# Kernel tuning notes

Measured on AMD Instinct MI355X. Metric: run time of the kernel, lower is better.

The kernel has to match this reference:

```python
import jax, jax.numpy as jnp
import numpy as np
import math

B, S, D, H = 2, 2048, 1024, 16
DK = D // H


def setup_inputs() -> dict:
    key = jax.random.key(0)
    ks = jax.random.split(key, 14)
    inp = {
        "query": jax.random.normal(ks[0], (B, S, D), dtype=jnp.float32),
        "key": jax.random.normal(ks[1], (B, S, D), dtype=jnp.float32),
        "value": jax.random.normal(ks[2], (B, S, D), dtype=jnp.float32),
        "group_prob": jax.random.uniform(ks[3], (B, S, S), dtype=jnp.float32),
        "mask": jax.random.randint(ks[4], (B, S), 0, 2, dtype=jnp.int32),
    }
    scale = 0.02
    inp["Wq"] = jax.random.normal(ks[5], (D, D), dtype=jnp.float32) * scale
    inp["bq"] = jnp.zeros((D,), dtype=jnp.float32)
    inp["Wk"] = jax.random.normal(ks[6], (D, D), dtype=jnp.float32) * scale
    inp["bk"] = jnp.zeros((D,), dtype=jnp.float32)
    inp["Wv"] = jax.random.normal(ks[7], (D, D), dtype=jnp.float32) * scale
    inp["bv"] = jnp.zeros((D,), dtype=jnp.float32)
    inp["Wo"] = jax.random.normal(ks[8], (D, D), dtype=jnp.float32) * scale
    inp["bo"] = jnp.zeros((D,), dtype=jnp.float32)
    return inp


def reference(query, key, value, group_prob, mask, Wq, bq, Wk, bk, Wv, bv, Wo, bo):
    b, s, d = query.shape
    # project and split heads: [B,S,D] -> [B,H,S,DK]
    def proj(x, W, bias):
        return (x @ W.T + bias).reshape(b, s, H, DK).transpose(0, 2, 1, 3)

    q = proj(query, Wq, bq)
    k = proj(key, Wk, bk)
    v = proj(value, Wv, bv)

    scores = jnp.einsum("bhqd,bhkd->bhqk", q, k) / math.sqrt(DK)  # [B,H,S,S]

    # combined mask: padding-row mask OR diagonal (always attend to self)
    eye = jnp.eye(s, dtype=jnp.int32)
    combined = mask[:, None, None, :] | eye[None, None, :, :]  # [B,1,S,S]
    scores = jnp.where(combined == 0, jnp.float32(-1e9), scores)

    p_attn = jax.nn.softmax(scores, axis=-1)
    p_attn = p_attn * group_prob[:, None, :, :]  # post-softmax group scaling

    x = jnp.einsum("bhqk,bhkd->bhqd", p_attn, v)  # [B,H,S,DK]
    x = x.transpose(0, 2, 1, 3).reshape(b, s, d)
    return x @ Wo.T + bo
```

## Files before the change

kernel.cpp:

```cpp
#include <hip/hip_runtime.h>
#include <hip/hip_bf16.h>
#include <stdint.h>

typedef __bf16 bf16x8 __attribute__((ext_vector_type(8)));
typedef float f32x4 __attribute__((ext_vector_type(4)));

__device__ __forceinline__ void gld16(const void* g, void* l) {
  __builtin_amdgcn_global_load_lds(
      (__attribute__((address_space(1))) void*)(uintptr_t)(g),
      (__attribute__((address_space(3))) void*)(l), 16, 0, 0);
}

struct CastArgs {
  const float* src[7];
  __bf16* dst[7];
  int n[7];
};

__global__ __launch_bounds__(256) void cast_bf16_kernel(CastArgs a) {
  const int t = blockIdx.y;
  const int i = (blockIdx.x * 256 + threadIdx.x) * 8;
  if (i >= a.n[t]) return;
  const float4* s = (const float4*)(a.src[t] + i);
  float4 v0 = s[0], v1 = s[1];
  bf16x8 o;
  o[0] = (__bf16)v0.x; o[1] = (__bf16)v0.y; o[2] = (__bf16)v0.z; o[3] = (__bf16)v0.w;
  o[4] = (__bf16)v1.x; o[5] = (__bf16)v1.y; o[6] = (__bf16)v1.z; o[7] = (__bf16)v1.w;
  *(bf16x8*)(a.dst[t] + i) = o;
}

__global__ __launch_bounds__(256) void cast_gp_kernel(const float* __restrict__ src,
                                                      __bf16* __restrict__ dst) {
  const int i = (blockIdx.x * 256 + threadIdx.x) * 8;
  const float4* s = (const float4*)(src + i);
  float4 v0 = s[0], v1 = s[1];
  bf16x8 o;
  o[0] = (__bf16)v0.x; o[1] = (__bf16)v0.y; o[2] = (__bf16)v0.z; o[3] = (__bf16)v0.w;
  o[4] = (__bf16)v1.x; o[5] = (__bf16)v1.y; o[6] = (__bf16)v1.z; o[7] = (__bf16)v1.w;
  *(bf16x8*)(dst + i) = o;
}

struct QkvArgs {
  const __bf16* A[3];
  const __bf16* B[3];
  const float* bias[3];
  __bf16* out[3];
};

__global__ __launch_bounds__(256) void qkv_gemm(QkvArgs args) {
  __shared__ __align__(16) __bf16 As[128 * 32];
  __shared__ __align__(16) __bf16 Bs[128 * 32];
  const int tid = threadIdx.x;
  const int z = blockIdx.y;
  const int bx = blockIdx.x;
  const int m0 = (z < 2 ? (bx >> 3) : (bx & 7)) * 128;
  const int n0 = (z < 2 ? (bx & 7) : (bx >> 3)) * 128;
  const __bf16* A = args.A[z];
  const __bf16* B = args.B[z];
  const float* bias = args.bias[z];
  __bf16* out = args.out[z];
  const float scale = (z == 0) ? 0.125f : 1.0f;

  const int lane = tid & 63, wid = tid >> 6;
  const int wm = (wid & 1) * 64, wn = (wid >> 1) * 64;
  const int l16 = lane & 15, quad = lane >> 4;

  const int sc = (tid & 3) ^ ((tid >> 2) & 3);
  const __bf16* ga = A + (size_t)(m0 + (tid >> 2)) * 1024 + sc * 8;
  const __bf16* gb = B + (size_t)(n0 + (tid >> 2)) * 1024 + sc * 8;
  char* lA = (char*)As + tid * 16;
  char* lB = (char*)Bs + tid * 16;
  const int a_off = (wm + l16) * 64 + ((quad ^ (l16 & 3)) * 16);
  const int b_off = (wn + l16) * 64 + ((quad ^ (l16 & 3)) * 16);

  f32x4 acc[4][4] = {};

  for (int k0 = 0; k0 < 1024; k0 += 32) {
    __syncthreads();
    gld16(ga + k0, lA);
    gld16(ga + k0 + 64 * 1024, lA + 4096);
    gld16(gb + k0, lB);
    gld16(gb + k0 + 64 * 1024, lB + 4096);
    __syncthreads();
    bf16x8 af[4], bfr[4];
#pragma unroll
    for (int mi = 0; mi < 4; ++mi)
      af[mi] = *(const bf16x8*)((const char*)As + a_off + mi * 1024);
#pragma unroll
    for (int ni = 0; ni < 4; ++ni)
      bfr[ni] = *(const bf16x8*)((const char*)Bs + b_off + ni * 1024);
#pragma unroll
    for (int mi = 0; mi < 4; ++mi)
#pragma unroll
      for (int ni = 0; ni < 4; ++ni)
        acc[mi][ni] = __builtin_amdgcn_mfma_f32_16x16x32_bf16(af[mi], bfr[ni],
                                                              acc[mi][ni], 0, 0, 0);
  }

  if (z < 2) {
#pragma unroll
    for (int ni = 0; ni < 4; ++ni) {
      const int col = n0 + wn + ni * 16 + l16;
      const int h = col >> 6, dk = col & 63;
      const float bb = bias[col];
#pragma unroll
      for (int mi = 0; mi < 4; ++mi)
#pragma unroll
        for (int r = 0; r < 4; ++r) {
          const int row = m0 + wm + mi * 16 + quad * 4 + r;
          const int b = row >> 11, s = row & 2047;
          out[((size_t)(b * 16 + h) * 2048 + s) * 64 + dk] =
              (__bf16)((acc[mi][ni][r] + bb) * scale);
        }
    }
  } else {
#pragma unroll
    for (int mi = 0; mi < 4; ++mi)
#pragma unroll
      for (int r = 0; r < 4; ++r) {
        const int rowm = m0 + wm + mi * 16 + quad * 4 + r;
        const int h = rowm >> 6, dk = rowm & 63;
        const float bb = bias[rowm];
#pragma unroll
        for (int ni = 0; ni < 4; ++ni) {
          const int coln = n0 + wn + ni * 16 + l16;
          const int b = coln >> 11, s = coln & 2047;
          out[((size_t)(b * 16 + h) * 64 + dk) * 2048 + s] =
              (__bf16)(acc[mi][ni][r] + bb);
        }
      }
  }
}

__global__ __launch_bounds__(256) void gemm_out(const __bf16* __restrict__ A,
                                                const __bf16* __restrict__ B,
                                                const float* __restrict__ bias,
                                                float* __restrict__ out) {
  __shared__ __align__(16) __bf16 As[128 * 32];
  __shared__ __align__(16) __bf16 Bs[128 * 32];
  const int tid = threadIdx.x;
  const int m0 = blockIdx.y * 128;
  const int n0 = blockIdx.x * 128;
  const int lane = tid & 63, wid = tid >> 6;
  const int wm = (wid & 1) * 64, wn = (wid >> 1) * 64;
  const int l16 = lane & 15, quad = lane >> 4;

  const int sc = (tid & 3) ^ ((tid >> 2) & 3);
  const __bf16* ga = A + (size_t)(m0 + (tid >> 2)) * 1024 + sc * 8;
  const __bf16* gb = B + (size_t)(n0 + (tid >> 2)) * 1024 + sc * 8;
  char* lA = (char*)As + tid * 16;
  char* lB = (char*)Bs + tid * 16;
  const int a_off = (wm + l16) * 64 + ((quad ^ (l16 & 3)) * 16);
  const int b_off = (wn + l16) * 64 + ((quad ^ (l16 & 3)) * 16);

  f32x4 acc[4][4] = {};

  for (int k0 = 0; k0 < 1024; k0 += 32) {
    __syncthreads();
    gld16(ga + k0, lA);
    gld16(ga + k0 + 64 * 1024, lA + 4096);
    gld16(gb + k0, lB);
    gld16(gb + k0 + 64 * 1024, lB + 4096);
    __syncthreads();
    bf16x8 af[4], bfr[4];
#pragma unroll
    for (int mi = 0; mi < 4; ++mi)
      af[mi] = *(const bf16x8*)((const char*)As + a_off + mi * 1024);
#pragma unroll
    for (int ni = 0; ni < 4; ++ni)
      bfr[ni] = *(const bf16x8*)((const char*)Bs + b_off + ni * 1024);
#pragma unroll
    for (int mi = 0; mi < 4; ++mi)
#pragma unroll
      for (int ni = 0; ni < 4; ++ni)
        acc[mi][ni] = __builtin_amdgcn_mfma_f32_16x16x32_bf16(af[mi], bfr[ni],
                                                              acc[mi][ni], 0, 0, 0);
  }

#pragma unroll
  for (int ni = 0; ni < 4; ++ni) {
    const int col = n0 + wn + ni * 16 + l16;
    const float bb = bias[col];
#pragma unroll
    for (int mi = 0; mi < 4; ++mi)
#pragma unroll
      for (int r = 0; r < 4; ++r) {
        const int row = m0 + wm + mi * 16 + quad * 4 + r;
        out[(size_t)row * 1024 + col] = acc[mi][ni][r] + bb;
      }
  }
}

__global__ __launch_bounds__(256) void attn_kernel(
    const __bf16* __restrict__ Qh, const __bf16* __restrict__ Kh,
    const __bf16* __restrict__ Vt, const __bf16* __restrict__ gp16,
    const int* __restrict__ maskp, __bf16* __restrict__ xb) {
  __shared__ __align__(16) __bf16 Qs[64 * 64];
  __shared__ __align__(16) __bf16 Ks[64 * 64];
  __shared__ __align__(16) __bf16 Vs[64 * 64];
  __shared__ __align__(16) __bf16 Ps[4][16 * 64];
  __shared__ unsigned long long mbits[32];

  const int tid = threadIdx.x;
  const int qt = blockIdx.x, bh = blockIdx.y;
  const int b = bh >> 4, h = bh & 15;
  const int q0 = qt * 64;
  const int lane = tid & 63, wid = tid >> 6, l16 = lane & 15, quad = lane >> 4;
  const size_t head_off = (size_t)bh * (2048 * 64);

  const int srow = tid >> 3;
  const int sc8 = (tid & 7) ^ (srow & 7);
  const int fxor = (l16 & 7);

  {
    const __bf16* gq = Qh + head_off + (size_t)(q0 + srow) * 64 + sc8 * 8;
    gld16(gq, (char*)Qs + tid * 16);
    gld16(gq + 32 * 64, (char*)Qs + 4096 + tid * 16);
  }
  {
    const int* mr = maskp + b * 2048;
#pragma unroll
    for (int t = 0; t < 8; ++t) {
      const int kt2 = wid * 8 + t;
      const int mv = mr[kt2 * 64 + lane];
      const unsigned long long bal = __ballot(mv != 0);
      if (lane == 0) mbits[kt2] = bal;
    }
  }
  __syncthreads();
  bf16x8 aq[2];
  aq[0] = *(const bf16x8*)((const char*)Qs + (wid * 16 + l16) * 128 +
                           ((quad ^ fxor) * 16));
  aq[1] = *(const bf16x8*)((const char*)Qs + (wid * 16 + l16) * 128 +
                           (((4 + quad) ^ fxor) * 16));

  f32x4 o[4] = {};
  float lp[4] = {0.f, 0.f, 0.f, 0.f};
  int irow[4];
#pragma unroll
  for (int r = 0; r < 4; ++r) irow[r] = q0 + wid * 16 + quad * 4 + r;

  const __bf16* gk0 = Kh + head_off + (size_t)srow * 64 + sc8 * 8;
  const __bf16* gv0 = Vt + head_off + (size_t)srow * 2048 + sc8 * 8;
  const __bf16* gpl = gp16 + (size_t)b * 2048 * 2048 +
                      (size_t)(q0 + wid * 16 + l16) * 2048 + quad * 8;

  for (int kt = 0; kt < 32; ++kt) {
    __syncthreads();
    gld16(gk0 + kt * 4096, (char*)Ks + tid * 16);
    gld16(gk0 + kt * 4096 + 2048, (char*)Ks + 4096 + tid * 16);
    gld16(gv0 + kt * 64, (char*)Vs + tid * 16);
    gld16(gv0 + kt * 64 + 32 * 2048, (char*)Vs + 4096 + tid * 16);

    bf16x8 g8_0 = *(const bf16x8*)(gpl + kt * 64);
    bf16x8 g8_1 = *(const bf16x8*)(gpl + kt * 64 + 32);

    const unsigned long long sh = mbits[kt] >> l16;
    const uint32_t shlo = (uint32_t)sh, shhi = (uint32_t)(sh >> 32);
    const bool mk[4] = {(shlo & 1) != 0, (shlo & 0x10000u) != 0,
                        (shhi & 1) != 0, (shhi & 0x10000u) != 0};
    __syncthreads();

    f32x4 sc[4] = {};
#pragma unroll
    for (int kh = 0; kh < 2; ++kh)
#pragma unroll
      for (int ni = 0; ni < 4; ++ni) {
        bf16x8 bk = *(const bf16x8*)((const char*)Ks + (ni * 16 + l16) * 128 +
                                     (((kh * 4 + quad) ^ fxor) * 16));
        sc[ni] = __builtin_amdgcn_mfma_f32_16x16x32_bf16(aq[kh], bk, sc[ni], 0, 0, 0);
      }

    float pw[4][4];
    if (kt != qt) {
#pragma unroll
      for (int ni = 0; ni < 4; ++ni)
#pragma unroll
        for (int r = 0; r < 4; ++r) {
          const float e = __expf(sc[ni][r]);
          const float p = mk[ni] ? e : 0.f;
          lp[r] += p;
          pw[ni][r] = p;
        }
    } else {
#pragma unroll
      for (int ni = 0; ni < 4; ++ni)
#pragma unroll
        for (int r = 0; r < 4; ++r) {
          const float e = __expf(sc[ni][r]);
          const bool diag = (ni == wid) && (l16 == quad * 4 + r);
          const float p = (mk[ni] || diag) ? e : 0.f;
          lp[r] += p;
          pw[ni][r] = p;
        }
    }

#pragma unroll
    for (int ni = 0; ni < 4; ++ni)
#pragma unroll
      for (int r = 0; r < 4; ++r) {
        const int prow = quad * 4 + r;
        const int pchunk = (ni * 2 + (l16 >> 3)) ^ (prow & 7);
        *(__bf16*)((char*)&Ps[wid][0] + prow * 128 + pchunk * 16 + (l16 & 7) * 2) =
            (__bf16)pw[ni][r];
      }
    asm volatile("s_waitcnt lgkmcnt(0)" ::: "memory");

#pragma unroll
    for (int kh = 0; kh < 2; ++kh) {
      bf16x8 ap = *(const bf16x8*)((const char*)&Ps[wid][0] + l16 * 128 +
                                   (((kh * 4 + quad) ^ fxor) * 16));
      const bf16x8 g8 = kh ? g8_1 : g8_0;
      bf16x8 apg;
#pragma unroll
      for (int j = 0; j < 8; ++j)
        apg[j] = (__bf16)((float)ap[j] * (float)g8[j]);
#pragma unroll
      for (int ni = 0; ni < 4; ++ni) {
        bf16x8 bv = *(const bf16x8*)((const char*)Vs + (ni * 16 + l16) * 128 +
                                     (((kh * 4 + quad) ^ fxor) * 16));
        o[ni] = __builtin_amdgcn_mfma_f32_16x16x32_bf16(apg, bv, o[ni], 0, 0, 0);
      }
    }
  }

#pragma unroll
  for (int r = 0; r < 4; ++r) {
    lp[r] += __shfl_xor(lp[r], 1);
    lp[r] += __shfl_xor(lp[r], 2);
    lp[r] += __shfl_xor(lp[r], 4);
    lp[r] += __shfl_xor(lp[r], 8);
    lp[r] = 1.f / lp[r];
  }
#pragma unroll
  for (int ni = 0; ni < 4; ++ni) {
    const int dk = ni * 16 + l16;
#pragma unroll
    for (int r = 0; r < 4; ++r) {
      const float val = o[ni][r] * lp[r];
      xb[((size_t)(b * 2048 + irow[r])) * 1024 + h * 64 + dk] = (__bf16)val;
    }
  }
}

extern "C" void kernel_launch(void* const* d_in, const int* in_sizes, int n_in,
                              void* d_out, int out_size, void* d_ws, size_t ws_size,
                              hipStream_t stream) {
  const float* query = (const float*)d_in[0];
  const float* key_  = (const float*)d_in[1];
  const float* value = (const float*)d_in[2];
  const float* gprob = (const float*)d_in[3];
  const int*   maskp = (const int*)d_in[4];
  const float* Wq = (const float*)d_in[5];
  const float* bq = (const float*)d_in[6];
  const float* Wk = (const float*)d_in[7];
  const float* bk = (const float*)d_in[8];
  const float* Wv = (const float*)d_in[9];
  const float* bv = (const float*)d_in[10];
  const float* Wo = (const float*)d_in[11];
  const float* bo = (const float*)d_in[12];

  char* ws = (char*)d_ws;
  const size_t MB = 1 << 20;
  __bf16* qb  = (__bf16*)(ws + 0 * MB);
  __bf16* kb  = (__bf16*)(ws + 8 * MB);
  __bf16* vb  = (__bf16*)(ws + 16 * MB);
  __bf16* Wqb = (__bf16*)(ws + 24 * MB);
  __bf16* Wkb = (__bf16*)(ws + 26 * MB);
  __bf16* Wvb = (__bf16*)(ws + 28 * MB);
  __bf16* Wob = (__bf16*)(ws + 30 * MB);
  __bf16* Qh  = (__bf16*)(ws + 32 * MB);
  __bf16* Kh  = (__bf16*)(ws + 40 * MB);
  __bf16* Vt  = (__bf16*)(ws + 48 * MB);
  __bf16* xb  = (__bf16*)(ws + 56 * MB);
  __bf16* gp16 = (__bf16*)(ws + 0 * MB);

  CastArgs ca;
  ca.src[0] = query; ca.dst[0] = qb;  ca.n[0] = 4194304;
  ca.src[1] = key_;  ca.dst[1] = kb;  ca.n[1] = 4194304;
  ca.src[2] = value; ca.dst[2] = vb;  ca.n[2] = 4194304;
  ca.src[3] = Wq;    ca.dst[3] = Wqb; ca.n[3] = 1048576;
  ca.src[4] = Wk;    ca.dst[4] = Wkb; ca.n[4] = 1048576;
  ca.src[5] = Wv;    ca.dst[5] = Wvb; ca.n[5] = 1048576;
  ca.src[6] = Wo;    ca.dst[6] = Wob; ca.n[6] = 1048576;
  cast_bf16_kernel<<<dim3(2048, 7), 256, 0, stream>>>(ca);

  QkvArgs qa;
  qa.A[0] = qb;  qa.B[0] = Wqb; qa.bias[0] = bq; qa.out[0] = Qh;
  qa.A[1] = kb;  qa.B[1] = Wkb; qa.bias[1] = bk; qa.out[1] = Kh;
  qa.A[2] = Wvb; qa.B[2] = vb;  qa.bias[2] = bv; qa.out[2] = Vt;
  qkv_gemm<<<dim3(256, 3), 256, 0, stream>>>(qa);

  cast_gp_kernel<<<dim3(4096), 256, 0, stream>>>(gprob, gp16);
  attn_kernel<<<dim3(32, 32), 256, 0, stream>>>(Qh, Kh, Vt, gp16, maskp, xb);
  gemm_out<<<dim3(8, 32), 256, 0, stream>>>(xb, Wob, bo, (float*)d_out);
}
```

Measured before the change: 333.5 us.

## Double-buffer K/V tiles, read fp32 group_prob directly, use exp2 with folded scale

The attention loop now double-buffers K and V tiles in LDS and prefetches the next tile and its group_prob values while computing the current one, leaving one barrier per iteration instead of two. The separate group_prob bf16 cast kernel is removed, so attention reads fp32 group_prob directly. This avoids a full write and re-read of the large matrix but doubles the bytes attention loads for it. The log2(e) factor is folded into the Q projection scale so exp2 replaces expf. The extra LDS buffers and prefetch registers may lower occupancy.

After: 323.8 us. 2.9% less time.

```diff
diff --git a/kernel.cpp b/kernel.cpp
--- a/kernel.cpp
+++ b/kernel.cpp
@@ -4,6 +4,8 @@
 
 typedef __bf16 bf16x8 __attribute__((ext_vector_type(8)));
 typedef float f32x4 __attribute__((ext_vector_type(4)));
+
+#define QSCALE 0.1803368801111244f
 
 __device__ __forceinline__ void gld16(const void* g, void* l) {
   __builtin_amdgcn_global_load_lds(
@@ -27,17 +29,6 @@
   o[0] = (__bf16)v0.x; o[1] = (__bf16)v0.y; o[2] = (__bf16)v0.z; o[3] = (__bf16)v0.w;
   o[4] = (__bf16)v1.x; o[5] = (__bf16)v1.y; o[6] = (__bf16)v1.z; o[7] = (__bf16)v1.w;
   *(bf16x8*)(a.dst[t] + i) = o;
-}
-
-__global__ __launch_bounds__(256) void cast_gp_kernel(const float* __restrict__ src,
-                                                      __bf16* __restrict__ dst) {
-  const int i = (blockIdx.x * 256 + threadIdx.x) * 8;
-  const float4* s = (const float4*)(src + i);
-  float4 v0 = s[0], v1 = s[1];
-  bf16x8 o;
-  o[0] = (__bf16)v0.x; o[1] = (__bf16)v0.y; o[2] = (__bf16)v0.z; o[3] = (__bf16)v0.w;
-  o[4] = (__bf16)v1.x; o[5] = (__bf16)v1.y; o[6] = (__bf16)v1.z; o[7] = (__bf16)v1.w;
-  *(bf16x8*)(dst + i) = o;
 }
 
 struct QkvArgs {
@@ -59,7 +50,7 @@
   const __bf16* B = args.B[z];
   const float* bias = args.bias[z];
   __bf16* out = args.out[z];
-  const float scale = (z == 0) ? 0.125f : 1.0f;
+  const float scale = (z == 0) ? QSCALE : 1.0f;
 
   const int lane = tid & 63, wid = tid >> 6;
   const int wm = (wid & 1) * 64, wn = (wid >> 1) * 64;
@@ -193,11 +184,11 @@
 
 __global__ __launch_bounds__(256) void attn_kernel(
     const __bf16* __restrict__ Qh, const __bf16* __restrict__ Kh,
-    const __bf16* __restrict__ Vt, const __bf16* __restrict__ gp16,
+    const __bf16* __restrict__ Vt, const float* __restrict__ gprob,
     const int* __restrict__ maskp, __bf16* __restrict__ xb) {
   __shared__ __align__(16) __bf16 Qs[64 * 64];
-  __shared__ __align__(16) __bf16 Ks[64 * 64];
-  __shared__ __align__(16) __bf16 Vs[64 * 64];
+  __shared__ __align__(16) __bf16 Ks[2][64 * 64];
+  __shared__ __align__(16) __bf16 Vs[2][64 * 64];
   __shared__ __align__(16) __bf16 Ps[4][16 * 64];
   __shared__ unsigned long long mbits[32];
 
@@ -212,10 +203,17 @@
   const int sc8 = (tid & 7) ^ (srow & 7);
   const int fxor = (l16 & 7);
 
+  const __bf16* gk0 = Kh + head_off + (size_t)srow * 64 + sc8 * 8;
+  const __bf16* gv0 = Vt + head_off + (size_t)srow * 2048 + sc8 * 8;
+
   {
     const __bf16* gq = Qh + head_off + (size_t)(q0 + srow) * 64 + sc8 * 8;
     gld16(gq, (char*)Qs + tid * 16);
     gld16(gq + 32 * 64, (char*)Qs + 4096 + tid * 16);
+    gld16(gk0, (char*)Ks + tid * 16);
+    gld16(gk0 + 2048, (char*)Ks + 4096 + tid * 16);
+    gld16(gv0, (char*)Vs + tid * 16);
+    gld16(gv0 + 32 * 2048, (char*)Vs + 4096 + tid * 16);
   }
   {
     const int* mr = maskp + b * 2048;
@@ -240,33 +238,41 @@
 #pragma unroll
   for (int r = 0; r < 4; ++r) irow[r] = q0 + wid * 16 + quad * 4 + r;
 
-  const __bf16* gk0 = Kh + head_off + (size_t)srow * 64 + sc8 * 8;
-  const __bf16* gv0 = Vt + head_off + (size_t)srow * 2048 + sc8 * 8;
-  const __bf16* gpl = gp16 + (size_t)b * 2048 * 2048 +
-                      (size_t)(q0 + wid * 16 + l16) * 2048 + quad * 8;
+  const float* gpl = gprob + (size_t)b * 2048 * 2048 +
+                     (size_t)(q0 + wid * 16 + l16) * 2048 + quad * 8;
+  float4 g0 = *(const float4*)(gpl);
+  float4 g1 = *(const float4*)(gpl + 4);
+  float4 g2 = *(const float4*)(gpl + 32);
+  float4 g3 = *(const float4*)(gpl + 36);
 
   for (int kt = 0; kt < 32; ++kt) {
-    __syncthreads();
-    gld16(gk0 + kt * 4096, (char*)Ks + tid * 16);
-    gld16(gk0 + kt * 4096 + 2048, (char*)Ks + 4096 + tid * 16);
-    gld16(gv0 + kt * 64, (char*)Vs + tid * 16);
-    gld16(gv0 + kt * 64 + 32 * 2048, (char*)Vs + 4096 + tid * 16);
-
-    bf16x8 g8_0 = *(const bf16x8*)(gpl + kt * 64);
-    bf16x8 g8_1 = *(const bf16x8*)(gpl + kt * 64 + 32);
+    const int cur = kt & 1;
+    float4 gn0, gn1, gn2, gn3;
+    if (kt < 31) {
+      const int nb = cur ^ 1;
+      gld16(gk0 + (kt + 1) * 4096, (char*)Ks + nb * 8192 + tid * 16);
+      gld16(gk0 + (kt + 1) * 4096 + 2048, (char*)Ks + nb * 8192 + 4096 + tid * 16);
+      gld16(gv0 + (kt + 1) * 64, (char*)Vs + nb * 8192 + tid * 16);
+      gld16(gv0 + (kt + 1) * 64 + 32 * 2048, (char*)Vs + nb * 8192 + 4096 + tid * 16);
+      const float* gn = gpl + (kt + 1) * 64;
+      gn0 = *(const float4*)(gn);
+      gn1 = *(const float4*)(gn + 4);
+      gn2 = *(const float4*)(gn + 32);
+      gn3 = *(const float4*)(gn + 36);
+    }
 
     const unsigned long long sh = mbits[kt] >> l16;
     const uint32_t shlo = (uint32_t)sh, shhi = (uint32_t)(sh >> 32);
     const bool mk[4] = {(shlo & 1) != 0, (shlo & 0x10000u) != 0,
                         (shhi & 1) != 0, (shhi & 0x10000u) != 0};
-    __syncthreads();
 
     f32x4 sc[4] = {};
 #pragma unroll
     for (int kh = 0; kh < 2; ++kh)
 #pragma unroll
       for (int ni = 0; ni < 4; ++ni) {
-        bf16x8 bk = *(const bf16x8*)((const char*)Ks + (ni * 16 + l16) * 128 +
+        bf16x8 bk = *(const bf16x8*)((const char*)Ks + cur * 8192 +
+                                     (ni * 16 + l16) * 128 +
                                      (((kh * 4 + quad) ^ fxor) * 16));
         sc[ni] = __builtin_amdgcn_mfma_f32_16x16x32_bf16(aq[kh], bk, sc[ni], 0, 0, 0);
       }
@@ -277,7 +283,7 @@
       for (int ni = 0; ni < 4; ++ni)
 #pragma unroll
         for (int r = 0; r < 4; ++r) {
-          const float e = __expf(sc[ni][r]);
+          const float e = __builtin_exp2f(sc[ni][r]);
           const float p = mk[ni] ? e : 0.f;
           lp[r] += p;
           pw[ni][r] = p;
@@ -287,7 +293,7 @@
       for (int ni = 0; ni < 4; ++ni)
 #pragma unroll
         for (int r = 0; r < 4; ++r) {
-          const float e = __expf(sc[ni][r]);
+          const float e = __builtin_exp2f(sc[ni][r]);
           const bool diag = (ni == wid) && (l16 == quad * 4 + r);
           const float p = (mk[ni] || diag) ? e : 0.f;
           lp[r] += p;
@@ -306,22 +312,27 @@
       }
     asm volatile("s_waitcnt lgkmcnt(0)" ::: "memory");
 
+    const float gfl[16] = {g0.x, g0.y, g0.z, g0.w, g1.x, g1.y, g1.z, g1.w,
+                           g2.x, g2.y, g2.z, g2.w, g3.x, g3.y, g3.z, g3.w};
 #pragma unroll
     for (int kh = 0; kh < 2; ++kh) {
       bf16x8 ap = *(const bf16x8*)((const char*)&Ps[wid][0] + l16 * 128 +
                                    (((kh * 4 + quad) ^ fxor) * 16));
-      const bf16x8 g8 = kh ? g8_1 : g8_0;
       bf16x8 apg;
 #pragma unroll
       for (int j = 0; j < 8; ++j)
-        apg[j] = (__bf16)((float)ap[j] * (float)g8[j]);
+        apg[j] = (__bf16)((float)ap[j] * gfl[kh * 8 + j]);
 #pragma unroll
       for (int ni = 0; ni < 4; ++ni) {
-        bf16x8 bv = *(const bf16x8*)((const char*)Vs + (ni * 16 + l16) * 128 +
+        bf16x8 bv = *(const bf16x8*)((const char*)Vs + cur * 8192 +
+                                     (ni * 16 + l16) * 128 +
                                      (((kh * 4 + quad) ^ fxor) * 16));
         o[ni] = __builtin_amdgcn_mfma_f32_16x16x32_bf16(apg, bv, o[ni], 0, 0, 0);
       }
     }
+
+    if (kt < 31) { g0 = gn0; g1 = gn1; g2 = gn2; g3 = gn3; }
+    __syncthreads();
   }
 
 #pragma unroll
@@ -373,7 +384,6 @@
   __bf16* Kh  = (__bf16*)(ws + 40 * MB);
   __bf16* Vt  = (__bf16*)(ws + 48 * MB);
   __bf16* xb  = (__bf16*)(ws + 56 * MB);
-  __bf16* gp16 = (__bf16*)(ws + 0 * MB);
 
   CastArgs ca;
   ca.src[0] = query; ca.dst[0] = qb;  ca.n[0] = 4194304;
@@ -391,7 +401,6 @@
   qa.A[2] = Wvb; qa.B[2] = vb;  qa.bias[2] = bv; qa.out[2] = Vt;
   qkv_gemm<<<dim3(256, 3), 256, 0, stream>>>(qa);
 
-  cast_gp_kernel<<<dim3(4096), 256, 0, stream>>>(gprob, gp16);
-  attn_kernel<<<dim3(32, 32), 256, 0, stream>>>(Qh, Kh, Vt, gp16, maskp, xb);
+  attn_kernel<<<dim3(32, 32), 256, 0, stream>>>(Qh, Kh, Vt, gprob, maskp, xb);
   gemm_out<<<dim3(8, 32), 256, 0, stream>>>(xb, Wob, bo, (float*)d_out);
 }
```

## Fuse group_prob cast into attention, switch to 32x32 MFMA with split-K waves

Applied to the files above, without the earlier changes.

Drops the separate group_prob fp32->bf16 cast kernel and reads fp32 group_prob directly inside the attention kernel, multiplying it into P in registers. The attention kernel is restructured to use 32x32x16 MFMAs with Q kept in registers, splitting each key tile across two waves and reducing partial outputs through LDS at the end. P is kept in registers via lane shuffles instead of being written to and read back from LDS. exp is replaced by exp2 with log2e folded into the Q scale. This removes a full pass over the large group_prob tensor and the P round trip through LDS, but doubles the group_prob bytes the attention kernel reads and adds an end-of-kernel reduction.

After: 341.2 us. +2.3%, slower.

```diff
diff --git a/kernel.cpp b/kernel.cpp
--- a/kernel.cpp
+++ b/kernel.cpp
@@ -4,11 +4,20 @@
 
 typedef __bf16 bf16x8 __attribute__((ext_vector_type(8)));
 typedef float f32x4 __attribute__((ext_vector_type(4)));
+typedef float f32x16 __attribute__((ext_vector_type(16)));
+
+#define QSCALE 0.1803368801111244f
 
 __device__ __forceinline__ void gld16(const void* g, void* l) {
   __builtin_amdgcn_global_load_lds(
       (__attribute__((address_space(1))) void*)(uintptr_t)(g),
       (__attribute__((address_space(3))) void*)(l), 16, 0, 0);
+}
+
+__device__ __forceinline__ uint32_t pk_bf16(float a, float b) {
+  union { __bf16 h[2]; uint32_t u; } t;
+  t.h[0] = (__bf16)a; t.h[1] = (__bf16)b;
+  return t.u;
 }
 
 struct CastArgs {
@@ -27,17 +36,6 @@
   o[0] = (__bf16)v0.x; o[1] = (__bf16)v0.y; o[2] = (__bf16)v0.z; o[3] = (__bf16)v0.w;
   o[4] = (__bf16)v1.x; o[5] = (__bf16)v1.y; o[6] = (__bf16)v1.z; o[7] = (__bf16)v1.w;
   *(bf16x8*)(a.dst[t] + i) = o;
-}
-
-__global__ __launch_bounds__(256) void cast_gp_kernel(const float* __restrict__ src,
-                                                      __bf16* __restrict__ dst) {
-  const int i = (blockIdx.x * 256 + threadIdx.x) * 8;
-  const float4* s = (const float4*)(src + i);
-  float4 v0 = s[0], v1 = s[1];
-  bf16x8 o;
-  o[0] = (__bf16)v0.x; o[1] = (__bf16)v0.y; o[2] = (__bf16)v0.z; o[3] = (__bf16)v0.w;
-  o[4] = (__bf16)v1.x; o[5] = (__bf16)v1.y; o[6] = (__bf16)v1.z; o[7] = (__bf16)v1.w;
-  *(bf16x8*)(dst + i) = o;
 }
 
 struct QkvArgs {
@@ -59,7 +57,7 @@
   const __bf16* B = args.B[z];
   const float* bias = args.bias[z];
   __bf16* out = args.out[z];
-  const float scale = (z == 0) ? 0.125f : 1.0f;
+  const float scale = (z == 0) ? QSCALE : 1.0f;
 
   const int lane = tid & 63, wid = tid >> 6;
   const int wm = (wid & 1) * 64, wn = (wid >> 1) * 64;
@@ -193,57 +191,52 @@
 
 __global__ __launch_bounds__(256) void attn_kernel(
     const __bf16* __restrict__ Qh, const __bf16* __restrict__ Kh,
-    const __bf16* __restrict__ Vt, const __bf16* __restrict__ gp16,
+    const __bf16* __restrict__ Vt, const float* __restrict__ gprob,
     const int* __restrict__ maskp, __bf16* __restrict__ xb) {
-  __shared__ __align__(16) __bf16 Qs[64 * 64];
   __shared__ __align__(16) __bf16 Ks[64 * 64];
   __shared__ __align__(16) __bf16 Vs[64 * 64];
-  __shared__ __align__(16) __bf16 Ps[4][16 * 64];
+  __shared__ float lps[2][64];
   __shared__ unsigned long long mbits[32];
 
   const int tid = threadIdx.x;
   const int qt = blockIdx.x, bh = blockIdx.y;
-  const int b = bh >> 4, h = bh & 15;
+  const int b = bh >> 4, h16 = bh & 15;
   const int q0 = qt * 64;
-  const int lane = tid & 63, wid = tid >> 6, l16 = lane & 15, quad = lane >> 4;
+  const int lane = tid & 63, wid = tid >> 6;
+  const int qw = wid & 1, kw = wid >> 1;
+  const int l32 = lane & 31, hh = lane >> 5;
   const size_t head_off = (size_t)bh * (2048 * 64);
 
   const int srow = tid >> 3;
   const int sc8 = (tid & 7) ^ (srow & 7);
-  const int fxor = (l16 & 7);
-
-  {
-    const __bf16* gq = Qh + head_off + (size_t)(q0 + srow) * 64 + sc8 * 8;
-    gld16(gq, (char*)Qs + tid * 16);
-    gld16(gq + 32 * 64, (char*)Qs + 4096 + tid * 16);
-  }
+  const int fx = l32 & 7;
+
+  const __bf16* gk0 = Kh + head_off + (size_t)srow * 64 + sc8 * 8;
+  const __bf16* gv0 = Vt + head_off + (size_t)srow * 2048 + sc8 * 8;
+
   {
     const int* mr = maskp + b * 2048;
 #pragma unroll
     for (int t = 0; t < 8; ++t) {
       const int kt2 = wid * 8 + t;
-      const int mv = mr[kt2 * 64 + lane];
-      const unsigned long long bal = __ballot(mv != 0);
+      const unsigned long long bal = __ballot(mr[kt2 * 64 + lane] != 0);
       if (lane == 0) mbits[kt2] = bal;
     }
   }
-  __syncthreads();
-  bf16x8 aq[2];
-  aq[0] = *(const bf16x8*)((const char*)Qs + (wid * 16 + l16) * 128 +
-                           ((quad ^ fxor) * 16));
-  aq[1] = *(const bf16x8*)((const char*)Qs + (wid * 16 + l16) * 128 +
-                           (((4 + quad) ^ fxor) * 16));
-
-  f32x4 o[4] = {};
-  float lp[4] = {0.f, 0.f, 0.f, 0.f};
-  int irow[4];
-#pragma unroll
-  for (int r = 0; r < 4; ++r) irow[r] = q0 + wid * 16 + quad * 4 + r;
-
-  const __bf16* gk0 = Kh + head_off + (size_t)srow * 64 + sc8 * 8;
-  const __bf16* gv0 = Vt + head_off + (size_t)srow * 2048 + sc8 * 8;
-  const __bf16* gpl = gp16 + (size_t)b * 2048 * 2048 +
-                      (size_t)(q0 + wid * 16 + l16) * 2048 + quad * 8;
+
+  const int qrow = q0 + qw * 32 + l32;
+  bf16x8 bq[4];
+  {
+    const __bf16* gq = Qh + head_off + (size_t)qrow * 64 + hh * 8;
+#pragma unroll
+    for (int dkb = 0; dkb < 4; ++dkb) bq[dkb] = *(const bf16x8*)(gq + dkb * 16);
+  }
+
+  f32x16 o0 = {}, o1 = {};
+  float lq[4] = {0.f, 0.f, 0.f, 0.f};
+
+  const float* gbase = gprob + ((size_t)b << 22) + (size_t)qrow * 2048 +
+                       kw * 32 + hh * 4;
 
   for (int kt = 0; kt < 32; ++kt) {
     __syncthreads();
@@ -252,94 +245,121 @@
     gld16(gv0 + kt * 64, (char*)Vs + tid * 16);
     gld16(gv0 + kt * 64 + 32 * 2048, (char*)Vs + 4096 + tid * 16);
 
-    bf16x8 g8_0 = *(const bf16x8*)(gpl + kt * 64);
-    bf16x8 g8_1 = *(const bf16x8*)(gpl + kt * 64 + 32);
-
-    const unsigned long long sh = mbits[kt] >> l16;
-    const uint32_t shlo = (uint32_t)sh, shhi = (uint32_t)(sh >> 32);
-    const bool mk[4] = {(shlo & 1) != 0, (shlo & 0x10000u) != 0,
-                        (shhi & 1) != 0, (shhi & 0x10000u) != 0};
-    __syncthreads();
-
-    f32x4 sc[4] = {};
-#pragma unroll
-    for (int kh = 0; kh < 2; ++kh)
-#pragma unroll
-      for (int ni = 0; ni < 4; ++ni) {
-        bf16x8 bk = *(const bf16x8*)((const char*)Ks + (ni * 16 + l16) * 128 +
-                                     (((kh * 4 + quad) ^ fxor) * 16));
-        sc[ni] = __builtin_amdgcn_mfma_f32_16x16x32_bf16(aq[kh], bk, sc[ni], 0, 0, 0);
-      }
-
-    float pw[4][4];
-    if (kt != qt) {
-#pragma unroll
-      for (int ni = 0; ni < 4; ++ni)
-#pragma unroll
-        for (int r = 0; r < 4; ++r) {
-          const float e = __expf(sc[ni][r]);
-          const float p = mk[ni] ? e : 0.f;
-          lp[r] += p;
-          pw[ni][r] = p;
-        }
+    f32x4 gvv[4];
+#pragma unroll
+    for (int gi = 0; gi < 4; ++gi)
+      gvv[gi] = *(const f32x4*)(gbase + kt * 64 + gi * 8);
+    const uint32_t mu =
+        (uint32_t)(mbits[kt] >> (kw * 32 + hh * 4));
+    __syncthreads();
+
+    f32x16 ssc = {};
+#pragma unroll
+    for (int dkb = 0; dkb < 4; ++dkb) {
+      const int row = kw * 32 + l32;
+      const int cc = (2 * dkb + hh) ^ fx;
+      bf16x8 ak = *(const bf16x8*)((const char*)Ks + (row << 7) + (cc << 4));
+      ssc = __builtin_amdgcn_mfma_f32_32x32x16_bf16(ak, bq[dkb], ssc, 0, 0, 0);
+    }
+
+    float pv[16];
+    if (!(kt == qt && qw == kw)) {
+#pragma unroll
+      for (int e = 0; e < 16; ++e) {
+        const int bi = (e & 3) + 8 * (e >> 2);
+        float p = __builtin_exp2f(ssc[e]);
+        p = ((mu >> bi) & 1) ? p : 0.f;
+        lq[e >> 2] += p;
+        pv[e] = p * gvv[e >> 2][e & 3];
+      }
     } else {
 #pragma unroll
-      for (int ni = 0; ni < 4; ++ni)
-#pragma unroll
-        for (int r = 0; r < 4; ++r) {
-          const float e = __expf(sc[ni][r]);
-          const bool diag = (ni == wid) && (l16 == quad * 4 + r);
-          const float p = (mk[ni] || diag) ? e : 0.f;
-          lp[r] += p;
-          pw[ni][r] = p;
-        }
-    }
-
-#pragma unroll
-    for (int ni = 0; ni < 4; ++ni)
-#pragma unroll
-      for (int r = 0; r < 4; ++r) {
-        const int prow = quad * 4 + r;
-        const int pchunk = (ni * 2 + (l16 >> 3)) ^ (prow & 7);
-        *(__bf16*)((char*)&Ps[wid][0] + prow * 128 + pchunk * 16 + (l16 & 7) * 2) =
-            (__bf16)pw[ni][r];
-      }
-    asm volatile("s_waitcnt lgkmcnt(0)" ::: "memory");
-
-#pragma unroll
-    for (int kh = 0; kh < 2; ++kh) {
-      bf16x8 ap = *(const bf16x8*)((const char*)&Ps[wid][0] + l16 * 128 +
-                                   (((kh * 4 + quad) ^ fxor) * 16));
-      const bf16x8 g8 = kh ? g8_1 : g8_0;
-      bf16x8 apg;
-#pragma unroll
-      for (int j = 0; j < 8; ++j)
-        apg[j] = (__bf16)((float)ap[j] * (float)g8[j]);
-#pragma unroll
-      for (int ni = 0; ni < 4; ++ni) {
-        bf16x8 bv = *(const bf16x8*)((const char*)Vs + (ni * 16 + l16) * 128 +
-                                     (((kh * 4 + quad) ^ fxor) * 16));
-        o[ni] = __builtin_amdgcn_mfma_f32_16x16x32_bf16(apg, bv, o[ni], 0, 0, 0);
-      }
-    }
-  }
-
-#pragma unroll
-  for (int r = 0; r < 4; ++r) {
-    lp[r] += __shfl_xor(lp[r], 1);
-    lp[r] += __shfl_xor(lp[r], 2);
-    lp[r] += __shfl_xor(lp[r], 4);
-    lp[r] += __shfl_xor(lp[r], 8);
-    lp[r] = 1.f / lp[r];
-  }
-#pragma unroll
-  for (int ni = 0; ni < 4; ++ni) {
-    const int dk = ni * 16 + l16;
-#pragma unroll
-    for (int r = 0; r < 4; ++r) {
-      const float val = o[ni][r] * lp[r];
-      xb[((size_t)(b * 2048 + irow[r])) * 1024 + h * 64 + dk] = (__bf16)val;
-    }
+      for (int e = 0; e < 16; ++e) {
+        const int bi = (e & 3) + 8 * (e >> 2);
+        float p = __builtin_exp2f(ssc[e]);
+        const bool m = (((mu >> bi) & 1) != 0) || (l32 == bi + 4 * hh);
+        p = m ? p : 0.f;
+        lq[e >> 2] += p;
+        pv[e] = p * gvv[e >> 2][e & 3];
+      }
+    }
+
+    uint32_t pr[8];
+#pragma unroll
+    for (int p8 = 0; p8 < 8; ++p8) pr[p8] = pk_bf16(pv[2 * p8], pv[2 * p8 + 1]);
+
+    bf16x8 pf[2];
+#pragma unroll
+    for (int ks = 0; ks < 2; ++ks) {
+      const uint32_t x0 = hh ? pr[4 * ks + 0] : pr[4 * ks + 2];
+      const uint32_t x1 = hh ? pr[4 * ks + 1] : pr[4 * ks + 3];
+      const uint32_t s0 = (uint32_t)__shfl_xor((int)x0, 32);
+      const uint32_t s1 = (uint32_t)__shfl_xor((int)x1, 32);
+      union { uint32_t u[4]; bf16x8 v; } U;
+      U.u[0] = hh ? s0 : pr[4 * ks + 0];
+      U.u[1] = hh ? s1 : pr[4 * ks + 1];
+      U.u[2] = hh ? pr[4 * ks + 2] : s0;
+      U.u[3] = hh ? pr[4 * ks + 3] : s1;
+      pf[ks] = U.v;
+    }
+
+#pragma unroll
+    for (int mb = 0; mb < 2; ++mb)
+#pragma unroll
+      for (int ks = 0; ks < 2; ++ks) {
+        const int row = mb * 32 + l32;
+        const int cc = (4 * kw + 2 * ks + hh) ^ fx;
+        bf16x8 av = *(const bf16x8*)((const char*)Vs + (row << 7) + (cc << 4));
+        if (mb == 0)
+          o0 = __builtin_amdgcn_mfma_f32_32x32x16_bf16(av, pf[ks], o0, 0, 0, 0);
+        else
+          o1 = __builtin_amdgcn_mfma_f32_32x32x16_bf16(av, pf[ks], o1, 0, 0, 0);
+      }
+  }
+
+  float lpq = (lq[0] + lq[1]) + (lq[2] + lq[3]);
+
+  __syncthreads();
+  if (kw == 1) {
+    char* cb = (char*)(qw ? (void*)Vs : (void*)Ks);
+#pragma unroll
+    for (int ch = 0; ch < 8; ++ch) {
+      const int mb = ch >> 2, e4 = ch & 3;
+      f32x4 w;
+#pragma unroll
+      for (int i = 0; i < 4; ++i) w[i] = (mb ? o1 : o0)[e4 * 4 + i];
+      *(f32x4*)(cb + lane * 128 + ((ch ^ (lane & 7)) << 4)) = w;
+    }
+    lps[qw][lane] = lpq;
+  }
+  __syncthreads();
+  if (kw == 0) {
+    const char* cb = (const char*)(qw ? (const void*)Vs : (const void*)Ks);
+#pragma unroll
+    for (int ch = 0; ch < 8; ++ch) {
+      const int mb = ch >> 2, e4 = ch & 3;
+      f32x4 w = *(const f32x4*)(cb + lane * 128 + ((ch ^ (lane & 7)) << 4));
+#pragma unroll
+      for (int i = 0; i < 4; ++i) {
+        if (mb) o1[e4 * 4 + i] += w[i];
+        else    o0[e4 * 4 + i] += w[i];
+      }
+    }
+    lpq += lps[qw][lane];
+    lpq += __shfl_xor(lpq, 32);
+    const float inv = 1.f / lpq;
+
+    __bf16* xrow = xb + ((size_t)(b * 2048 + qrow)) * 1024 + h16 * 64;
+#pragma unroll
+    for (int mb = 0; mb < 2; ++mb)
+#pragma unroll
+      for (int rg = 0; rg < 4; ++rg) {
+        const f32x16& oo = mb ? o1 : o0;
+        uint2 ww;
+        ww.x = pk_bf16(oo[rg * 4 + 0] * inv, oo[rg * 4 + 1] * inv);
+        ww.y = pk_bf16(oo[rg * 4 + 2] * inv, oo[rg * 4 + 3] * inv);
+        *(uint2*)(xrow + mb * 32 + rg * 8 + hh * 4) = ww;
+      }
   }
 }
 
@@ -373,7 +393,6 @@
   __bf16* Kh  = (__bf16*)(ws + 40 * MB);
   __bf16* Vt  = (__bf16*)(ws + 48 * MB);
   __bf16* xb  = (__bf16*)(ws + 56 * MB);
-  __bf16* gp16 = (__bf16*)(ws + 0 * MB);
 
   CastArgs ca;
   ca.src[0] = query; ca.dst[0] = qb;  ca.n[0] = 4194304;
@@ -391,7 +410,6 @@
   qa.A[2] = Wvb; qa.B[2] = vb;  qa.bias[2] = bv; qa.out[2] = Vt;
   qkv_gemm<<<dim3(256, 3), 256, 0, stream>>>(qa);
 
-  cast_gp_kernel<<<dim3(4096), 256, 0, stream>>>(gprob, gp16);
-  attn_kernel<<<dim3(32, 32), 256, 0, stream>>>(Qh, Kh, Vt, gp16, maskp, xb);
+  attn_kernel<<<dim3(32, 32), 256, 0, stream>>>(Qh, Kh, Vt, gprob, maskp, xb);
   gemm_out<<<dim3(8, 32), 256, 0, stream>>>(xb, Wob, bo, (float*)d_out);
 }
```
